# Kernel tuning notes

Measured on AMD Instinct MI355X. Metric: run time of the kernel, lower is better.

## Reference

```python
import jax, jax.numpy as jnp
import numpy as np

N_NODES = 50000
N_EDGES = 800000
IN_DIM = 128
HID = 128
N_LAYERS = 3


def setup_inputs() -> dict:
    key = jax.random.key(0)
    ks = jax.random.split(key, 12)
    x = jax.random.normal(ks[0], (N_NODES, IN_DIM), dtype=jnp.float32)
    edge_index = jax.random.randint(ks[1], (2, N_EDGES), 0, N_NODES, dtype=jnp.int64)
    s = 1.0 / np.sqrt(HID)
    # per-conv 2-layer MLP weights, stacked over layers (all dims equal since in=hidden)
    W_a = jax.random.uniform(ks[2], (N_LAYERS, HID, HID), jnp.float32, -s, s)
    b_a = jax.random.uniform(ks[3], (N_LAYERS, HID), jnp.float32, -s, s)
    W_b = jax.random.uniform(ks[4], (N_LAYERS, HID, HID), jnp.float32, -s, s)
    b_b = jax.random.uniform(ks[5], (N_LAYERS, HID), jnp.float32, -s, s)
    eps = jnp.zeros((N_LAYERS,), jnp.float32)  # train_eps=True, init 0
    W_h1 = jax.random.uniform(ks[6], (HID, HID // 2), jnp.float32, -s, s)
    b_h1 = jax.random.uniform(ks[7], (HID // 2,), jnp.float32, -s, s)
    s2 = 1.0 / np.sqrt(HID // 2)
    W_h2 = jax.random.uniform(ks[8], (HID // 2, 2), jnp.float32, -s2, s2)
    b_h2 = jax.random.uniform(ks[9], (2,), jnp.float32, -s2, s2)
    return {"x": x, "edge_index": edge_index, "eps": eps, "W_a": W_a, "b_a": b_a,
            "W_b": W_b, "b_b": b_b, "W_h1": W_h1, "b_h1": b_h1, "W_h2": W_h2, "b_h2": b_h2}


def reference(x, edge_index, eps, W_a, b_a, W_b, b_b, W_h1, b_h1, W_h2, b_h2):
    # Dropout is identity in eval mode. use_residual=False, use_input_mlp=False.
    src, dst = edge_index[0], edge_index[1]
    h = x.astype(jnp.float32)
    n = h.shape[0]
    for l in range(N_LAYERS):
        # GINConv: scatter-add of neighbor (source) features into target nodes
        agg = jax.ops.segment_sum(h[src], dst, num_segments=n)  # [N, H]
        z = (1.0 + eps[l]) * h + agg
        z = jnp.maximum(z @ W_a[l] + b_a[l], 0.0) @ W_b[l] + b_b[l]
        h = jnp.maximum(z, 0.0)  # outer ReLU after conv
    hid = jnp.maximum(h @ W_h1 + b_h1, 0.0)
    return hid @ W_h2 + b_h2  # [N, 2]
```

## Files before the change

kernel.cpp:

```cpp
#include <hip/hip_runtime.h>
#include <hip/hip_bf16.h>

#define N_NODES 50000
#define N_EDGES 800000
#define HID 128

#define NB 391
#define NBLK 160
#define EPB 5000

typedef __attribute__((ext_vector_type(8))) short short8;
typedef __attribute__((ext_vector_type(4))) float f32x4;
typedef __attribute__((ext_vector_type(4))) unsigned short us4;
typedef _Float16 hv8 __attribute__((ext_vector_type(8)));
typedef _Float16 hv4 __attribute__((ext_vector_type(4)));

__device__ __forceinline__ unsigned short f2bf(float v) {
    union { float f; unsigned u; } x; x.f = v;
    unsigned r = x.u + 0x7fff + ((x.u >> 16) & 1);
    return (unsigned short)(r >> 16);
}
__device__ __forceinline__ float bf2f(unsigned short b) {
    union { unsigned u; float f; } x; x.u = ((unsigned)b) << 16;
    return x.f;
}


__global__ __launch_bounds__(256)
void hist_k(const int* __restrict__ dst, int* __restrict__ bh, int E) {
    __shared__ int h[NB];
    for (int i = threadIdx.x; i < NB; i += 256) h[i] = 0;
    __syncthreads();
    const int base = blockIdx.x * EPB;
    const int end = min(base + EPB, E);
    for (int i = base + threadIdx.x; i < end; i += 256)
        atomicAdd(&h[dst[i] >> 7], 1);
    __syncthreads();
    for (int i = threadIdx.x; i < NB; i += 256)
        bh[i * NBLK + blockIdx.x] = h[i];
}

__global__ __launch_bounds__(256)
void scanA_k(const int* __restrict__ in, int* __restrict__ bsum, int n) {
    const int t = threadIdx.x, base = blockIdx.x * 2048 + t * 8;
    int s = 0;
#pragma unroll
    for (int k = 0; k < 8; ++k) s += (base + k < n) ? in[base + k] : 0;
    __shared__ int sh[256];
    sh[t] = s;
    __syncthreads();
    for (int o = 128; o > 0; o >>= 1) {
        if (t < o) sh[t] += sh[t + o];
        __syncthreads();
    }
    if (t == 0) bsum[blockIdx.x] = sh[0];
}

__global__ __launch_bounds__(256)
void scanC_k(const int* __restrict__ in, const int* __restrict__ bsum,
             int* __restrict__ out, int n, int B) {
    const int t = threadIdx.x, base = blockIdx.x * 2048 + t * 8;
    __shared__ int blockoff;
    if (t == 0) {
        int p = 0;
        for (int i = 0; i < blockIdx.x; ++i) p += bsum[i];
        blockoff = p;
    }
    int v[8]; int s = 0;
#pragma unroll
    for (int k = 0; k < 8; ++k) { v[k] = (base + k < n) ? in[base + k] : 0; s += v[k]; }
    __shared__ int sh[256];
    sh[t] = s;
    __syncthreads();
    for (int o = 1; o < 256; o <<= 1) {
        int u = (t >= o) ? sh[t - o] : 0;
        __syncthreads();
        sh[t] += u;
        __syncthreads();
    }
    int run = ((t == 0) ? 0 : sh[t - 1]) + blockoff;
#pragma unroll
    for (int k = 0; k < 8; ++k) {
        if (base + k < n) out[base + k] = run;
        run += v[k];
    }
}

__global__ __launch_bounds__(256)
void scatter_k(const int* __restrict__ src, const int* __restrict__ dst,
               const int* __restrict__ bhs, int* __restrict__ tmp, int E) {
    __shared__ int cur[NB];
    for (int i = threadIdx.x; i < NB; i += 256) cur[i] = bhs[i * NBLK + blockIdx.x];
    __syncthreads();
    const int base = blockIdx.x * EPB;
    const int end = min(base + EPB, E);
    for (int i = base + threadIdx.x; i < end; i += 256) {
        int d = dst[i];
        int p = atomicAdd(&cur[d >> 7], 1);
        tmp[p] = (src[i] << 7) | (d & 127);
    }
}

__global__ __launch_bounds__(256)
void bucket_k(const int* __restrict__ tmp, const int* __restrict__ bhs,
              int* __restrict__ offs, int* __restrict__ csr, int E, int N) {
    const int b = blockIdx.x;
    const int t = threadIdx.x;
    __shared__ int hist[128], excl[128], cur[128];
    const int bstart = bhs[b * NBLK];
    const int bend = (b + 1 < NB) ? bhs[(b + 1) * NBLK] : E;
    if (t < 128) hist[t] = 0;
    __syncthreads();
    for (int i = bstart + t; i < bend; i += 256)
        atomicAdd(&hist[tmp[i] & 127], 1);
    __syncthreads();
    if (t < 128) excl[t] = hist[t];
    __syncthreads();
    for (int o = 1; o < 128; o <<= 1) {
        int u = (t < 128 && t >= o) ? excl[t - o] : 0;
        __syncthreads();
        if (t < 128) excl[t] += u;
        __syncthreads();
    }
    const int node0 = b * 128;
    if (t < 128) {
        int base = bstart + ((t == 0) ? 0 : excl[t - 1]);
        if (node0 + t < N) offs[node0 + t] = base;
        cur[t] = base;
    }
    if (b == 0 && t == 0) offs[N] = E;
    __syncthreads();
    for (int i = bstart + t; i < bend; i += 256) {
        int e = tmp[i];
        int p = atomicAdd(&cur[e & 127], 1);
        csr[p] = e >> 7;
    }
}

#define XB 6250
#define WB 416
__global__ __launch_bounds__(256)
void cvt_k(const float* __restrict__ x, _Float16* __restrict__ xh,
           const float* __restrict__ Wa, const float* __restrict__ Wb,
           const float* __restrict__ Wh1,
           unsigned short* __restrict__ whi, unsigned short* __restrict__ wlo) {
    if (blockIdx.x < XB) {
        int i = blockIdx.x * 256 + threadIdx.x;
        if (i < 1600000) {
            float4 v = *(const float4*)&x[i * 4];
            hv4 o;
            o.x = (_Float16)v.x; o.y = (_Float16)v.y;
            o.z = (_Float16)v.z; o.w = (_Float16)v.w;
            *(hv4*)&xh[i * 4] = o;
        }
        return;
    }
    int id = (blockIdx.x - XB) * 256 + threadIdx.x;
    float v; int dst;
    if (id < 49152) {
        int l = id >> 14, e = id & 16383;
        v = Wa[id];
        int n = e & 127, k = e >> 7;
        dst = (2 * l) * 16384 + n * 128 + k;
    } else if (id < 98304) {
        int id2 = id - 49152;
        int l = id2 >> 14, e = id2 & 16383;
        v = Wb[id2];
        int n = e & 127, k = e >> 7;
        dst = (2 * l + 1) * 16384 + n * 128 + k;
    } else if (id < 106496) {
        int e = id - 98304;
        v = Wh1[e];
        int n = e & 63, k = e >> 6;
        dst = 6 * 16384 + n * 128 + k;
    } else return;
    unsigned short hi = f2bf(v);
    whi[dst] = hi;
    wlo[dst] = f2bf(v - bf2f(hi));
}

__global__ __launch_bounds__(256)
void agg16_k(const _Float16* __restrict__ h_in,
             const int* __restrict__ offs, const int* __restrict__ csr,
             const float* __restrict__ eps, int layer,
             _Float16* __restrict__ z) {
    const int qw = threadIdx.x >> 4;
    const int l16 = threadIdx.x & 15;
    const int node = blockIdx.x * 16 + qw;
    if (node >= N_NODES) return;
    const hv8* __restrict__ h8 = (const hv8*)h_in;
    const float sc = 1.0f + eps[layer];
    const int beg = offs[node], end = offs[node + 1];
    float a0[8] = {0,0,0,0,0,0,0,0};
    float a1[8] = {0,0,0,0,0,0,0,0};
    int j = beg;
    for (; j + 4 <= end; j += 4) {
        int s0 = csr[j], s1 = csr[j+1], s2 = csr[j+2], s3 = csr[j+3];
        hv8 v0 = h8[(size_t)s0 * 16 + l16];
        hv8 v1 = h8[(size_t)s1 * 16 + l16];
        hv8 v2 = h8[(size_t)s2 * 16 + l16];
        hv8 v3 = h8[(size_t)s3 * 16 + l16];
#pragma unroll
        for (int e = 0; e < 8; ++e) {
            a0[e] += (float)v0[e] + (float)v2[e];
            a1[e] += (float)v1[e] + (float)v3[e];
        }
    }
    for (; j < end; ++j) {
        hv8 v = h8[(size_t)csr[j] * 16 + l16];
#pragma unroll
        for (int e = 0; e < 8; ++e) a0[e] += (float)v[e];
    }
    hv8 self = h8[(size_t)node * 16 + l16];
    hv8 o;
#pragma unroll
    for (int e = 0; e < 8; ++e)
        o[e] = (_Float16)(sc * (float)self[e] + (a0[e] + a1[e]));
    ((hv8*)z)[(size_t)node * 16 + l16] = o;
}

template <bool HEAD>
__global__ __launch_bounds__(256)
void mlp_k(const _Float16* __restrict__ z_in,
           const unsigned short* __restrict__ WAhi, const unsigned short* __restrict__ WAlo,
           const float* __restrict__ ba,
           const unsigned short* __restrict__ WBhi, const unsigned short* __restrict__ WBlo,
           const float* __restrict__ bb,
           const unsigned short* __restrict__ WHhi, const unsigned short* __restrict__ WHlo,
           const float* __restrict__ bh1,
           const float* __restrict__ W2, const float* __restrict__ b2,
           void* __restrict__ outp) {
    __shared__ unsigned short Zhi[32 * 136];
    __shared__ unsigned short Zlo[32 * 136];
    const int t = threadIdx.x;
    const int wave = t >> 6, lane = t & 63;
    const int m = lane & 15, quad = lane >> 4;
    const int row0 = blockIdx.x * 32;

    {
        const int quart = lane >> 4, l16 = lane & 15;
        const hv8* __restrict__ z8 = (const hv8*)z_in;
        for (int g = 0; g < 2; ++g) {
            const int r = wave * 8 + g * 4 + quart;
            const int node = row0 + r;
            float o[8] = {0,0,0,0,0,0,0,0};
            if (node < N_NODES) {
                hv8 v = z8[(size_t)node * 16 + l16];
#pragma unroll
                for (int e = 0; e < 8; ++e) o[e] = (float)v[e];
            }
            us4 hi0, hi1, lo0, lo1;
#pragma unroll
            for (int e = 0; e < 4; ++e) {
                hi0[e] = f2bf(o[e]);     lo0[e] = f2bf(o[e]     - bf2f(hi0[e]));
                hi1[e] = f2bf(o[e + 4]); lo1[e] = f2bf(o[e + 4] - bf2f(hi1[e]));
            }
            *(us4*)&Zhi[r * 136 + l16 * 8]     = hi0;
            *(us4*)&Zhi[r * 136 + l16 * 8 + 4] = hi1;
            *(us4*)&Zlo[r * 136 + l16 * 8]     = lo0;
            *(us4*)&Zlo[r * 136 + l16 * 8 + 4] = lo1;
        }
    }
    __syncthreads();

    const int n0 = (wave * 32 + m) * 128 + quad * 8;
    const int n1 = (wave * 32 + 16 + m) * 128 + quad * 8;

    f32x4 acc[2][2];
    for (int s = 0; s < 2; ++s)
        for (int ct = 0; ct < 2; ++ct) acc[s][ct] = (f32x4){0, 0, 0, 0};
#pragma unroll 1
    for (int ks = 0; ks < 4; ++ks) {
        const int wo = ks * 32;
        short8 wh0 = *(const short8*)&WAhi[n0 + wo];
        short8 wl0 = *(const short8*)&WAlo[n0 + wo];
        short8 wh1 = *(const short8*)&WAhi[n1 + wo];
        short8 wl1 = *(const short8*)&WAlo[n1 + wo];
#pragma unroll
        for (int s = 0; s < 2; ++s) {
            const int r = s * 16 + m;
            short8 zh = *(const short8*)&Zhi[r * 136 + wo + quad * 8];
            short8 zl = *(const short8*)&Zlo[r * 136 + wo + quad * 8];
            acc[s][0] = __builtin_amdgcn_mfma_f32_16x16x32_bf16(zh, wh0, acc[s][0], 0, 0, 0);
            acc[s][0] = __builtin_amdgcn_mfma_f32_16x16x32_bf16(zh, wl0, acc[s][0], 0, 0, 0);
            acc[s][0] = __builtin_amdgcn_mfma_f32_16x16x32_bf16(zl, wh0, acc[s][0], 0, 0, 0);
            acc[s][1] = __builtin_amdgcn_mfma_f32_16x16x32_bf16(zh, wh1, acc[s][1], 0, 0, 0);
            acc[s][1] = __builtin_amdgcn_mfma_f32_16x16x32_bf16(zh, wl1, acc[s][1], 0, 0, 0);
            acc[s][1] = __builtin_amdgcn_mfma_f32_16x16x32_bf16(zl, wh1, acc[s][1], 0, 0, 0);
        }
    }
    __syncthreads();

    for (int s = 0; s < 2; ++s) {
        for (int ct = 0; ct < 2; ++ct) {
            int c = wave * 32 + ct * 16 + m;
            float bac = ba[c];
            for (int i = 0; i < 4; ++i) {
                int r = s * 16 + quad * 4 + i;
                float v = fmaxf(acc[s][ct][i] + bac, 0.0f);
                unsigned short hv = f2bf(v);
                Zhi[r * 136 + c] = hv;
                Zlo[r * 136 + c] = f2bf(v - bf2f(hv));
            }
        }
    }
    __syncthreads();

    for (int s = 0; s < 2; ++s)
        for (int ct = 0; ct < 2; ++ct) acc[s][ct] = (f32x4){0, 0, 0, 0};
#pragma unroll 1
    for (int ks = 0; ks < 4; ++ks) {
        const int wo = ks * 32;
        short8 wh0 = *(const short8*)&WBhi[n0 + wo];
        short8 wl0 = *(const short8*)&WBlo[n0 + wo];
        short8 wh1 = *(const short8*)&WBhi[n1 + wo];
        short8 wl1 = *(const short8*)&WBlo[n1 + wo];
#pragma unroll
        for (int s = 0; s < 2; ++s) {
            const int r = s * 16 + m;
            short8 zh = *(const short8*)&Zhi[r * 136 + wo + quad * 8];
            short8 zl = *(const short8*)&Zlo[r * 136 + wo + quad * 8];
            acc[s][0] = __builtin_amdgcn_mfma_f32_16x16x32_bf16(zh, wh0, acc[s][0], 0, 0, 0);
            acc[s][0] = __builtin_amdgcn_mfma_f32_16x16x32_bf16(zh, wl0, acc[s][0], 0, 0, 0);
            acc[s][0] = __builtin_amdgcn_mfma_f32_16x16x32_bf16(zl, wh0, acc[s][0], 0, 0, 0);
            acc[s][1] = __builtin_amdgcn_mfma_f32_16x16x32_bf16(zh, wh1, acc[s][1], 0, 0, 0);
            acc[s][1] = __builtin_amdgcn_mfma_f32_16x16x32_bf16(zh, wl1, acc[s][1], 0, 0, 0);
            acc[s][1] = __builtin_amdgcn_mfma_f32_16x16x32_bf16(zl, wh1, acc[s][1], 0, 0, 0);
        }
    }

    if (!HEAD) {
        _Float16* hout = (_Float16*)outp;
        for (int s = 0; s < 2; ++s) {
            for (int ct = 0; ct < 2; ++ct) {
                int c = wave * 32 + ct * 16 + m;
                float bbc = bb[c];
                for (int i = 0; i < 4; ++i) {
                    int row = row0 + s * 16 + quad * 4 + i;
                    if (row < N_NODES)
                        hout[(size_t)row * 128 + c] = (_Float16)fmaxf(acc[s][ct][i] + bbc, 0.0f);
                }
            }
        }
    } else {
        __syncthreads();

        for (int s = 0; s < 2; ++s) {
            for (int ct = 0; ct < 2; ++ct) {
                int c = wave * 32 + ct * 16 + m;
                float bbc = bb[c];
                for (int i = 0; i < 4; ++i) {
                    int r = s * 16 + quad * 4 + i;
                    float v = fmaxf(acc[s][ct][i] + bbc, 0.0f);
                    unsigned short hv = f2bf(v);
                    Zhi[r * 136 + c] = hv;
                    Zlo[r * 136 + c] = f2bf(v - bf2f(hv));
                }
            }
        }
        __syncthreads();

        const int nh = (wave * 16 + m) * 128 + quad * 8;
        f32x4 a3[2];
        for (int s = 0; s < 2; ++s) a3[s] = (f32x4){0, 0, 0, 0};
#pragma unroll 1
        for (int ks = 0; ks < 4; ++ks) {
            const int wo = ks * 32;
            short8 hh = *(const short8*)&WHhi[nh + wo];
            short8 hl = *(const short8*)&WHlo[nh + wo];
#pragma unroll
            for (int s = 0; s < 2; ++s) {
                const int r = s * 16 + m;
                short8 zh = *(const short8*)&Zhi[r * 136 + wo + quad * 8];
                short8 zl = *(const short8*)&Zlo[r * 136 + wo + quad * 8];
                a3[s] = __builtin_amdgcn_mfma_f32_16x16x32_bf16(zh, hh, a3[s], 0, 0, 0);
                a3[s] = __builtin_amdgcn_mfma_f32_16x16x32_bf16(zh, hl, a3[s], 0, 0, 0);
                a3[s] = __builtin_amdgcn_mfma_f32_16x16x32_bf16(zl, hh, a3[s], 0, 0, 0);
            }
        }
        __syncthreads();

        float* Hid = (float*)Zhi;
        for (int s = 0; s < 2; ++s) {
            int c = wave * 16 + m;
            float bc = bh1[c];
            for (int i = 0; i < 4; ++i) {
                int r = s * 16 + quad * 4 + i;
                Hid[r * 68 + c] = fmaxf(a3[s][i] + bc, 0.0f);
            }
        }
        __syncthreads();

        float* Red = (float*)Zlo;
        {
            int pair = t >> 2, seg = t & 3;
            int r = pair >> 1, col = pair & 1;
            float p = 0.0f;
#pragma unroll
            for (int j = seg * 16; j < seg * 16 + 16; ++j)
                p += Hid[r * 68 + j] * W2[j * 2 + col];
            Red[t] = p;
        }
        __syncthreads();
        if (t < 64) {
            float* outF = (float*)outp;
            int r = t >> 1, col = t & 1;
            float a = b2[col] + ((Red[t * 4] + Red[t * 4 + 1]) + (Red[t * 4 + 2] + Red[t * 4 + 3]));
            int node = row0 + r;
            if (node < N_NODES) outF[(size_t)node * 2 + col] = a;
        }
    }
}


extern "C" void kernel_launch(void* const* d_in, const int* in_sizes, int n_in,
                              void* d_out, int out_size, void* d_ws, size_t ws_size,
                              hipStream_t stream) {
    const float* x    = (const float*)d_in[0];
    const int*   ei   = (const int*)d_in[1];
    const float* eps  = (const float*)d_in[2];
    const float* W_a  = (const float*)d_in[3];
    const float* b_a  = (const float*)d_in[4];
    const float* W_b  = (const float*)d_in[5];
    const float* b_b  = (const float*)d_in[6];
    const float* W_h1 = (const float*)d_in[7];
    const float* b_h1 = (const float*)d_in[8];
    const float* W_h2 = (const float*)d_in[9];
    const float* b_h2 = (const float*)d_in[10];
    float* out = (float*)d_out;

    const int N = N_NODES, E = N_EDGES;
    const int* src = ei;
    const int* dst = ei + E;

    char* ws = (char*)d_ws;
    size_t off = 0;
    auto carve = [&](size_t bytes) {
        char* p = ws + off;
        off = (off + bytes + 255) & ~(size_t)255;
        return p;
    };
    _Float16* xh   = (_Float16*)carve((size_t)N * HID * sizeof(_Float16));
    _Float16* zb   = (_Float16*)carve((size_t)N * HID * sizeof(_Float16));
    _Float16* bufA = (_Float16*)carve((size_t)N * HID * sizeof(_Float16));
    _Float16* bufB = (_Float16*)carve((size_t)N * HID * sizeof(_Float16));
    int*   tmp    = (int*)carve((size_t)E * sizeof(int));
    int*   csr    = (int*)carve((size_t)E * sizeof(int));
    int*   offs   = (int*)carve((size_t)(N + 1) * sizeof(int));
    int*   bh     = (int*)carve((size_t)NB * NBLK * sizeof(int));
    int*   bhs    = (int*)carve((size_t)NB * NBLK * sizeof(int));
    int*   bsum   = (int*)carve(64 * sizeof(int));
    unsigned short* whi = (unsigned short*)carve(7 * 16384 * sizeof(unsigned short));
    unsigned short* wlo = (unsigned short*)carve(7 * 16384 * sizeof(unsigned short));
    (void)ws_size;

    const int M = NB * NBLK;
    const int SB = (M + 2047) / 2048;
    hist_k<<<NBLK, 256, 0, stream>>>(dst, bh, E);
    scanA_k<<<SB, 256, 0, stream>>>(bh, bsum, M);
    scanC_k<<<SB, 256, 0, stream>>>(bh, bsum, bhs, M, SB);
    scatter_k<<<NBLK, 256, 0, stream>>>(src, dst, bhs, tmp, E);
    bucket_k<<<NB, 256, 0, stream>>>(tmp, bhs, offs, csr, E, N);

    cvt_k<<<XB + WB, 256, 0, stream>>>(x, xh, W_a, W_b, W_h1, whi, wlo);

    const int agg_grid = (N + 15) / 16;
    const int mlp_grid = (N + 31) / 32;
    #define WSLOT(s) (whi + (s) * 16384), (wlo + (s) * 16384)
    #define NOHEAD (const unsigned short*)nullptr, (const unsigned short*)nullptr, \
                   (const float*)nullptr, (const float*)nullptr, (const float*)nullptr

    agg16_k<<<agg_grid, 256, 0, stream>>>(xh, offs, csr, eps, 0, zb);
    mlp_k<false><<<mlp_grid, 256, 0, stream>>>(zb, WSLOT(0), b_a + 0 * 128,
        WSLOT(1), b_b + 0 * 128, NOHEAD, (void*)bufA);
    agg16_k<<<agg_grid, 256, 0, stream>>>(bufA, offs, csr, eps, 1, zb);
    mlp_k<false><<<mlp_grid, 256, 0, stream>>>(zb, WSLOT(2), b_a + 1 * 128,
        WSLOT(3), b_b + 1 * 128, NOHEAD, (void*)bufB);
    agg16_k<<<agg_grid, 256, 0, stream>>>(bufB, offs, csr, eps, 2, zb);
    mlp_k<true><<<mlp_grid, 256, 0, stream>>>(zb, WSLOT(4), b_a + 2 * 128,
        WSLOT(5), b_b + 2 * 128, WSLOT(6), b_h1, W_h2, b_h2, (void*)out);
}
```

Baseline: 324.2 us.

## Double MLP row tile to 64 and pre-swizzle weights into MFMA fragment order

Measured after the change: 275.8 us. -14.9%, faster.

```diff
diff --git a/kernel.cpp b/kernel.cpp
--- a/kernel.cpp
+++ b/kernel.cpp
@@ -157,22 +157,23 @@
     }
     int id = (blockIdx.x - XB) * 256 + threadIdx.x;
     float v; int dst;
-    if (id < 49152) {
-        int l = id >> 14, e = id & 16383;
-        v = Wa[id];
-        int n = e & 127, k = e >> 7;
-        dst = (2 * l) * 16384 + n * 128 + k;
-    } else if (id < 98304) {
-        int id2 = id - 49152;
+    if (id < 98304) {
+        int isB = (id >= 49152);
+        int id2 = isB ? id - 49152 : id;
         int l = id2 >> 14, e = id2 & 16383;
-        v = Wb[id2];
-        int n = e & 127, k = e >> 7;
-        dst = (2 * l + 1) * 16384 + n * 128 + k;
+        v = isB ? Wb[id2] : Wa[id2];
+        int k = e >> 7, n = e & 127;
+        int w = n >> 5, ct = (n >> 4) & 1, m = n & 15;
+        int ks = k >> 5, quad = (k >> 3) & 3, j = k & 7;
+        int within = ((w * 8 + ks * 2 + ct) * 64 + quad * 16 + m) * 8 + j;
+        dst = (2 * l + isB) * 16384 + within;
     } else if (id < 106496) {
         int e = id - 98304;
         v = Wh1[e];
-        int n = e & 63, k = e >> 6;
-        dst = 6 * 16384 + n * 128 + k;
+        int k = e >> 6, n = e & 63;
+        int w = n >> 4, m = n & 15;
+        int ks = k >> 5, quad = (k >> 3) & 3, j = k & 7;
+        dst = 6 * 16384 + ((w * 4 + ks) * 64 + quad * 16 + m) * 8 + j;
     } else return;
     unsigned short hi = f2bf(v);
     whi[dst] = hi;
@@ -230,18 +231,18 @@
            const float* __restrict__ bh1,
            const float* __restrict__ W2, const float* __restrict__ b2,
            void* __restrict__ outp) {
-    __shared__ unsigned short Zhi[32 * 136];
-    __shared__ unsigned short Zlo[32 * 136];
+    __shared__ unsigned short Zhi[64 * 136];
+    __shared__ unsigned short Zlo[64 * 136];
     const int t = threadIdx.x;
     const int wave = t >> 6, lane = t & 63;
     const int m = lane & 15, quad = lane >> 4;
-    const int row0 = blockIdx.x * 32;
+    const int row0 = blockIdx.x * 64;
 
     {
         const int quart = lane >> 4, l16 = lane & 15;
         const hv8* __restrict__ z8 = (const hv8*)z_in;
-        for (int g = 0; g < 2; ++g) {
-            const int r = wave * 8 + g * 4 + quart;
+        for (int g = 0; g < 4; ++g) {
+            const int r = wave * 16 + g * 4 + quart;
             const int node = row0 + r;
             float o[8] = {0,0,0,0,0,0,0,0};
             if (node < N_NODES) {
@@ -263,24 +264,22 @@
     }
     __syncthreads();
 
-    const int n0 = (wave * 32 + m) * 128 + quad * 8;
-    const int n1 = (wave * 32 + 16 + m) * 128 + quad * 8;
-
-    f32x4 acc[2][2];
-    for (int s = 0; s < 2; ++s)
+    f32x4 acc[4][2];
+    for (int s = 0; s < 4; ++s)
         for (int ct = 0; ct < 2; ++ct) acc[s][ct] = (f32x4){0, 0, 0, 0};
 #pragma unroll 1
     for (int ks = 0; ks < 4; ++ks) {
-        const int wo = ks * 32;
-        short8 wh0 = *(const short8*)&WAhi[n0 + wo];
-        short8 wl0 = *(const short8*)&WAlo[n0 + wo];
-        short8 wh1 = *(const short8*)&WAhi[n1 + wo];
-        short8 wl1 = *(const short8*)&WAlo[n1 + wo];
-#pragma unroll
-        for (int s = 0; s < 2; ++s) {
+        const int fA = (wave * 8 + ks * 2) * 512 + lane * 8;
+        short8 wh0 = *(const short8*)&WAhi[fA];
+        short8 wl0 = *(const short8*)&WAlo[fA];
+        short8 wh1 = *(const short8*)&WAhi[fA + 512];
+        short8 wl1 = *(const short8*)&WAlo[fA + 512];
+        const int wo = ks * 32 + quad * 8;
+#pragma unroll
+        for (int s = 0; s < 4; ++s) {
             const int r = s * 16 + m;
-            short8 zh = *(const short8*)&Zhi[r * 136 + wo + quad * 8];
-            short8 zl = *(const short8*)&Zlo[r * 136 + wo + quad * 8];
+            short8 zh = *(const short8*)&Zhi[r * 136 + wo];
+            short8 zl = *(const short8*)&Zlo[r * 136 + wo];
             acc[s][0] = __builtin_amdgcn_mfma_f32_16x16x32_bf16(zh, wh0, acc[s][0], 0, 0, 0);
             acc[s][0] = __builtin_amdgcn_mfma_f32_16x16x32_bf16(zh, wl0, acc[s][0], 0, 0, 0);
             acc[s][0] = __builtin_amdgcn_mfma_f32_16x16x32_bf16(zl, wh0, acc[s][0], 0, 0, 0);
@@ -291,7 +290,7 @@
     }
     __syncthreads();
 
-    for (int s = 0; s < 2; ++s) {
+    for (int s = 0; s < 4; ++s) {
         for (int ct = 0; ct < 2; ++ct) {
             int c = wave * 32 + ct * 16 + m;
             float bac = ba[c];
@@ -306,20 +305,21 @@
     }
     __syncthreads();
 
-    for (int s = 0; s < 2; ++s)
+    for (int s = 0; s < 4; ++s)
         for (int ct = 0; ct < 2; ++ct) acc[s][ct] = (f32x4){0, 0, 0, 0};
 #pragma unroll 1
     for (int ks = 0; ks < 4; ++ks) {
-        const int wo = ks * 32;
-        short8 wh0 = *(const short8*)&WBhi[n0 + wo];
-        short8 wl0 = *(const short8*)&WBlo[n0 + wo];
-        short8 wh1 = *(const short8*)&WBhi[n1 + wo];
-        short8 wl1 = *(const short8*)&WBlo[n1 + wo];
-#pragma unroll
-        for (int s = 0; s < 2; ++s) {
+        const int fB = (wave * 8 + ks * 2) * 512 + lane * 8;
+        short8 wh0 = *(const short8*)&WBhi[fB];
+        short8 wl0 = *(const short8*)&WBlo[fB];
+        short8 wh1 = *(const short8*)&WBhi[fB + 512];
+        short8 wl1 = *(const short8*)&WBlo[fB + 512];
+        const int wo = ks * 32 + quad * 8;
+#pragma unroll
+        for (int s = 0; s < 4; ++s) {
             const int r = s * 16 + m;
-            short8 zh = *(const short8*)&Zhi[r * 136 + wo + quad * 8];
-            short8 zl = *(const short8*)&Zlo[r * 136 + wo + quad * 8];
+            short8 zh = *(const short8*)&Zhi[r * 136 + wo];
+            short8 zl = *(const short8*)&Zlo[r * 136 + wo];
             acc[s][0] = __builtin_amdgcn_mfma_f32_16x16x32_bf16(zh, wh0, acc[s][0], 0, 0, 0);
             acc[s][0] = __builtin_amdgcn_mfma_f32_16x16x32_bf16(zh, wl0, acc[s][0], 0, 0, 0);
             acc[s][0] = __builtin_amdgcn_mfma_f32_16x16x32_bf16(zl, wh0, acc[s][0], 0, 0, 0);
@@ -331,7 +331,7 @@
 
     if (!HEAD) {
         _Float16* hout = (_Float16*)outp;
-        for (int s = 0; s < 2; ++s) {
+        for (int s = 0; s < 4; ++s) {
             for (int ct = 0; ct < 2; ++ct) {
                 int c = wave * 32 + ct * 16 + m;
                 float bbc = bb[c];
@@ -345,7 +345,7 @@
     } else {
         __syncthreads();
 
-        for (int s = 0; s < 2; ++s) {
+        for (int s = 0; s < 4; ++s) {
             for (int ct = 0; ct < 2; ++ct) {
                 int c = wave * 32 + ct * 16 + m;
                 float bbc = bb[c];
@@ -360,19 +360,19 @@
         }
         __syncthreads();
 
-        const int nh = (wave * 16 + m) * 128 + quad * 8;
-        f32x4 a3[2];
-        for (int s = 0; s < 2; ++s) a3[s] = (f32x4){0, 0, 0, 0};
+        f32x4 a3[4];
+        for (int s = 0; s < 4; ++s) a3[s] = (f32x4){0, 0, 0, 0};
 #pragma unroll 1
         for (int ks = 0; ks < 4; ++ks) {
-            const int wo = ks * 32;
-            short8 hh = *(const short8*)&WHhi[nh + wo];
-            short8 hl = *(const short8*)&WHlo[nh + wo];
-#pragma unroll
-            for (int s = 0; s < 2; ++s) {
+            const int fH = (wave * 4 + ks) * 512 + lane * 8;
+            short8 hh = *(const short8*)&WHhi[fH];
+            short8 hl = *(const short8*)&WHlo[fH];
+            const int wo = ks * 32 + quad * 8;
+#pragma unroll
+            for (int s = 0; s < 4; ++s) {
                 const int r = s * 16 + m;
-                short8 zh = *(const short8*)&Zhi[r * 136 + wo + quad * 8];
-                short8 zl = *(const short8*)&Zlo[r * 136 + wo + quad * 8];
+                short8 zh = *(const short8*)&Zhi[r * 136 + wo];
+                short8 zl = *(const short8*)&Zlo[r * 136 + wo];
                 a3[s] = __builtin_amdgcn_mfma_f32_16x16x32_bf16(zh, hh, a3[s], 0, 0, 0);
                 a3[s] = __builtin_amdgcn_mfma_f32_16x16x32_bf16(zh, hl, a3[s], 0, 0, 0);
                 a3[s] = __builtin_amdgcn_mfma_f32_16x16x32_bf16(zl, hh, a3[s], 0, 0, 0);
@@ -381,7 +381,7 @@
         __syncthreads();
 
         float* Hid = (float*)Zhi;
-        for (int s = 0; s < 2; ++s) {
+        for (int s = 0; s < 4; ++s) {
             int c = wave * 16 + m;
             float bc = bh1[c];
             for (int i = 0; i < 4; ++i) {
@@ -393,19 +393,19 @@
 
         float* Red = (float*)Zlo;
         {
-            int pair = t >> 2, seg = t & 3;
+            int pair = t >> 1, seg = t & 1;
             int r = pair >> 1, col = pair & 1;
             float p = 0.0f;
 #pragma unroll
-            for (int j = seg * 16; j < seg * 16 + 16; ++j)
+            for (int j = seg * 32; j < seg * 32 + 32; ++j)
                 p += Hid[r * 68 + j] * W2[j * 2 + col];
             Red[t] = p;
         }
         __syncthreads();
-        if (t < 64) {
+        if (t < 128) {
             float* outF = (float*)outp;
             int r = t >> 1, col = t & 1;
-            float a = b2[col] + ((Red[t * 4] + Red[t * 4 + 1]) + (Red[t * 4 + 2] + Red[t * 4 + 3]));
+            float a = b2[col] + (Red[t * 2] + Red[t * 2 + 1]);
             int node = row0 + r;
             if (node < N_NODES) outF[(size_t)node * 2 + col] = a;
         }
@@ -465,7 +465,7 @@
     cvt_k<<<XB + WB, 256, 0, stream>>>(x, xh, W_a, W_b, W_h1, whi, wlo);
 
     const int agg_grid = (N + 15) / 16;
-    const int mlp_grid = (N + 31) / 32;
+    const int mlp_grid = (N + 63) / 64;
     #define WSLOT(s) (whi + (s) * 16384), (wlo + (s) * 16384)
     #define NOHEAD (const unsigned short*)nullptr, (const unsigned short*)nullptr, \
                    (const float*)nullptr, (const float*)nullptr, (const float*)nullptr
```
